# Performance work log

Measured on AMD Instinct MI355X. Metric: run time of the kernel, lower is better.

The kernel has to match this reference:

```python
import jax, jax.numpy as jnp
import numpy as np


def setup_inputs() -> dict:
    key = jax.random.key(0)
    kc, kh, kx, kwx, kwh = jax.random.split(key, 5)
    B, T, D, H = 64, 512, 1024, 1024
    c0 = jax.random.normal(kc, (B, H), dtype=jnp.float32)
    h0 = jax.random.normal(kh, (B, H), dtype=jnp.float32)
    xs = jax.random.normal(kx, (B, T, D), dtype=jnp.float32)
    # fan-in scaled init like lecun_normal (flax default)
    Wx = jax.random.normal(kwx, (D, 4 * H), dtype=jnp.float32) / np.sqrt(D)
    Wh = jax.random.normal(kwh, (H, 4 * H), dtype=jnp.float32) / np.sqrt(H)
    b = jnp.zeros((4 * H,), dtype=jnp.float32)
    return {"c0": c0, "h0": h0, "xs": xs, "Wx": Wx, "Wh": Wh, "b": b}


def _lstm(c0, h0, xs, Wx, Wh, b):
    # Batch the input-to-hidden projection across all timesteps (compute-dense GEMM)
    xproj = jnp.einsum('btd,dh->tbh', xs, Wx)  # [T, B, 4H], time-major for scan

    def step(carry, xp):
        c, h = carry
        gates = xp + h @ Wh + b                # [B, 4H]
        i, f, g, o = jnp.split(gates, 4, axis=-1)  # flax gate order: i, f, g, o
        new_c = jax.nn.sigmoid(f) * c + jax.nn.sigmoid(i) * jnp.tanh(g)
        new_h = jax.nn.sigmoid(o) * jnp.tanh(new_c)
        return (new_c, new_h), new_h

    (cT, hT), ys = jax.lax.scan(step, (c0, h0), xproj)
    return (cT, hT), jnp.transpose(ys, (1, 0, 2))  # ys back to [B, T, H]


def reference(c0, h0, xs, Wx, Wh, b):
    return _lstm(c0, h0, xs, Wx, Wh, b)
```

## Files before the change

### kernel.cpp

```cpp
#include <hip/hip_runtime.h>


typedef _Float16 half8 __attribute__((ext_vector_type(8)));
typedef float floatx4 __attribute__((ext_vector_type(4)));

__device__ __forceinline__ void gll16(const void* g, void* l) {
  __builtin_amdgcn_global_load_lds(
      (const __attribute__((address_space(1))) unsigned int*)g,
      (__attribute__((address_space(3))) unsigned int*)l, 16, 0, 0);
}

__device__ __forceinline__ float sigm(float x) { return 1.f / (1.f + __expf(-x)); }
__device__ __forceinline__ float tanhfast(float x) { return 1.f - 2.f / (__expf(2.f * x) + 1.f); }

__global__ void prep_ew(const float* __restrict__ xs, const float* __restrict__ h0,
                        _Float16* __restrict__ xs16, _Float16* __restrict__ hb0,
                        int* __restrict__ flags) {
  long gid = (long)blockIdx.x * blockDim.x + threadIdx.x;
  if (gid < 4194304) {
    const float4* p = (const float4*)xs + gid * 2;
    float4 u = p[0], w = p[1];
    half8 o;
    o[0] = (_Float16)u.x; o[1] = (_Float16)u.y; o[2] = (_Float16)u.z; o[3] = (_Float16)u.w;
    o[4] = (_Float16)w.x; o[5] = (_Float16)w.y; o[6] = (_Float16)w.z; o[7] = (_Float16)w.w;
    long e = gid * 8;
    long row = e >> 10;
    long b = row >> 9, t = row & 511;
    *(half8*)(xs16 + ((t << 6) + b) * 1024 + (e & 1023)) = o;
  } else if (gid < 4202496) {
    long j = gid - 4194304;
    const float4* p = (const float4*)h0 + j * 2;
    float4 u = p[0], w = p[1];
    half8 o;
    o[0] = (_Float16)u.x; o[1] = (_Float16)u.y; o[2] = (_Float16)u.z; o[3] = (_Float16)u.w;
    o[4] = (_Float16)w.x; o[5] = (_Float16)w.y; o[6] = (_Float16)w.z; o[7] = (_Float16)w.w;
    *(half8*)(hb0 + j * 8) = o;
  } else if (gid < 4203264) {
    flags[gid - 4202496] = 0;
  }
}

__global__ void transpose_k(const float* __restrict__ in, _Float16* __restrict__ outp) {
  __shared__ float s[32][33];
  int bx = blockIdx.x * 32, by = blockIdx.y * 32;
  int tx = threadIdx.x, ty = threadIdx.y;
#pragma unroll
  for (int k = 0; k < 32; k += 8)
    s[ty + k][tx] = in[(long)(by + ty + k) * 4096 + bx + tx];
  __syncthreads();
#pragma unroll
  for (int k = 0; k < 32; k += 8)
    outp[(long)(bx + ty + k) * 1024 + by + tx] = (_Float16)s[tx][ty + k];
}

__global__ __launch_bounds__(256, 1) void fused(const _Float16* __restrict__ xs16,
                                                const _Float16* __restrict__ wxt,
                                                _Float16* __restrict__ xprj,
                                                const _Float16* __restrict__ wht,
                                                const float* __restrict__ bias,
                                                const float* __restrict__ c0,
                                                _Float16* __restrict__ hbuf,
                                                int* __restrict__ flags,
                                                float* __restrict__ out) {
  __shared__ char smem[131072];
  const int tid = threadIdx.x;
  int* const cnt = flags + 256;
  int* const tot = flags + 512;

  if (blockIdx.x >= 64) {
    _Float16* sA = (_Float16*)smem;
    _Float16* sB = (_Float16*)(smem + 8192);
    const int gid = blockIdx.x - 64;
    const int by = gid >> 5, bx = gid & 31;
    const int w = tid >> 6, l = tid & 63, li = l & 15, q = l >> 4;
    const int wr = w >> 1, wc = w & 1;
    const int m0 = by * 128, n0 = bx * 128;
    floatx4 acc[4][4] = {};
    const _Float16* gA0 = xs16 + (long)(m0 + (w * 16 + li)) * 1024 + q * 8;
    const _Float16* gA1 = xs16 + (long)(m0 + ((4 + w) * 16 + li)) * 1024 + q * 8;
    const _Float16* gB0 = wxt + (long)(n0 + (w * 16 + li)) * 1024 + q * 8;
    const _Float16* gB1 = wxt + (long)(n0 + ((4 + w) * 16 + li)) * 1024 + q * 8;
    _Float16* lA0 = sA + (w * 64) * 8;
    _Float16* lA1 = sA + (256 + w * 64) * 8;
    _Float16* lB0 = sB + (w * 64) * 8;
    _Float16* lB1 = sB + (256 + w * 64) * 8;
    for (int k0 = 0; k0 < 1024; k0 += 32) {
      __syncthreads();
      gll16(gA0 + k0, lA0);
      gll16(gA1 + k0, lA1);
      gll16(gB0 + k0, lB0);
      gll16(gB1 + k0, lB1);
      __syncthreads();
      half8 af[4], bf[4];
      const half8* pA = (const half8*)sA;
      const half8* pB = (const half8*)sB;
#pragma unroll
      for (int i = 0; i < 4; i++) af[i] = pA[(wr * 4 + i) * 64 + l];
#pragma unroll
      for (int j = 0; j < 4; j++) bf[j] = pB[(wc * 4 + j) * 64 + l];
#pragma unroll
      for (int i = 0; i < 4; i++)
#pragma unroll
        for (int j = 0; j < 4; j++)
          acc[i][j] = __builtin_amdgcn_mfma_f32_16x16x32_f16(af[i], bf[j], acc[i][j], 0, 0, 0);
    }
#pragma unroll
    for (int i = 0; i < 4; i++) {
#pragma unroll
      for (int r = 0; r < 4; r++) {
        int m = m0 + wr * 64 + i * 16 + q * 4 + r;
#pragma unroll
        for (int j = 0; j < 4; j++) {
          int gn = n0 + wc * 64 + j * 16 + li;
          xprj[(long)m * 4096 + gn] = (_Float16)acc[i][j][r];
        }
      }
    }
    __syncthreads();
    if (tid == 0) {
      __builtin_amdgcn_fence(__ATOMIC_RELEASE, "agent");
      __hip_atomic_fetch_add(&cnt[by], 1, __ATOMIC_RELAXED, __HIP_MEMORY_SCOPE_AGENT);
      __hip_atomic_fetch_add(tot, 1, __ATOMIC_RELAXED, __HIP_MEMORY_SCOPE_AGENT);
    }
    return;
  }

  _Float16* sW = (_Float16*)smem;
  const int wgid = blockIdx.x;
  const int v = tid >> 6;
  const int l = tid & 63, li = l & 15, q = l >> 4;
  const int ks = wgid * 16;

#pragma unroll 4
  for (int i = 0; i < 32; i++) {
    int c = i * 256 + tid;
    int g = c >> 11, kk = (c >> 6) & 31;
    int cli = c & 15, cq = (c >> 4) & 3;
    gll16(wht + (long)((g << 10) + ks + cli) * 1024 + kk * 32 + cq * 8,
          sW + (long)(c - l) * 8);
  }
  float creg[4];
#pragma unroll
  for (int r = 0; r < 4; r++)
    creg[r] = c0[(long)(v * 16 + q * 4 + r) * 1024 + ks + li];
  float bs[4];
#pragma unroll
  for (int g = 0; g < 4; g++) bs[g] = bias[(g << 10) + ks + li];
  __syncthreads();

  const half8* pW = (const half8*)sW;
  const int fidx = 4 * l + v;
  int xdone = 0;

  for (int t = 0; t < 512; t++) {
    if (!xdone && !(t & 1)) {
      const int nb = t >> 1;
      for (;;) {
        int cr = __hip_atomic_load(&cnt[nb], __ATOMIC_RELAXED, __HIP_MEMORY_SCOPE_AGENT);
        if (cr >= 32) break;
        __builtin_amdgcn_s_sleep(16);
      }
      xdone = (__hip_atomic_load(tot, __ATOMIC_RELAXED, __HIP_MEMORY_SCOPE_AGENT) >= 8192);
      __builtin_amdgcn_fence(__ATOMIC_ACQUIRE, "agent");
    }

    const _Float16* xpt = xprj + (long)t * 262144 + ks + li;
    _Float16 xv[4][4];
#pragma unroll
    for (int g = 0; g < 4; g++)
#pragma unroll
      for (int r = 0; r < 4; r++)
        xv[g][r] = xpt[(long)(v * 16 + q * 4 + r) * 4096 + (g << 10)];

    for (;;) {
      int f = __hip_atomic_load(&flags[fidx], __ATOMIC_RELAXED, __HIP_MEMORY_SCOPE_AGENT);
      if (__all(f >= t)) break;
      __builtin_amdgcn_s_sleep(1);
    }
    __builtin_amdgcn_fence(__ATOMIC_ACQUIRE, "workgroup");

    const _Float16* hrow = hbuf + (long)t * 65536 + (long)(v * 16 + li) * 1024 + q * 8;
    floatx4 acc[4] = {};
    half8 ap[8];
#pragma unroll
    for (int p = 0; p < 8; p++) ap[p] = *(const half8*)(hrow + p * 32);
#pragma unroll
    for (int kk = 0; kk < 32; kk++) {
      half8 a = ap[kk & 7];
#pragma unroll
      for (int g = 0; g < 4; g++)
        acc[g] = __builtin_amdgcn_mfma_f32_16x16x32_f16(a, pW[((g * 32 + kk) << 6) + l], acc[g], 0, 0, 0);
      if (kk < 24) ap[kk & 7] = *(const half8*)(hrow + (kk + 8) * 32);
    }

    _Float16* hnext = hbuf + (long)(t + 1) * 65536;
    float hval[4], cval[4];
#pragma unroll
    for (int r = 0; r < 4; r++) {
      float gi = acc[0][r] + (float)xv[0][r] + bs[0];
      float gf = acc[1][r] + (float)xv[1][r] + bs[1];
      float gg = acc[2][r] + (float)xv[2][r] + bs[2];
      float go = acc[3][r] + (float)xv[3][r] + bs[3];
      float cN = sigm(gf) * creg[r] + sigm(gi) * tanhfast(gg);
      creg[r] = cN;
      cval[r] = cN;
      float hN = sigm(go) * tanhfast(cN);
      hval[r] = hN;
      int b = v * 16 + q * 4 + r;
      unsigned short hu = __builtin_bit_cast(unsigned short, (_Float16)hN);
      __hip_atomic_store((unsigned short*)hnext + (long)b * 1024 + ks + li, hu,
                         __ATOMIC_RELAXED, __HIP_MEMORY_SCOPE_AGENT);
    }
    __builtin_amdgcn_s_waitcnt(0);
    if (l == 0)
      __hip_atomic_store(&flags[4 * wgid + v], t + 1, __ATOMIC_RELAXED, __HIP_MEMORY_SCOPE_AGENT);

#pragma unroll
    for (int r = 0; r < 4; r++) {
      int b = v * 16 + q * 4 + r;
      out[131072 + (long)b * 524288 + (long)t * 1024 + ks + li] = hval[r];
      if (t == 511) {
        out[(long)b * 1024 + ks + li] = cval[r];
        out[65536 + (long)b * 1024 + ks + li] = hval[r];
      }
    }
  }
}

extern "C" void kernel_launch(void* const* d_in, const int* in_sizes, int n_in,
                              void* d_out, int out_size, void* d_ws, size_t ws_size,
                              hipStream_t stream) {
  const float* c0 = (const float*)d_in[0];
  const float* h0 = (const float*)d_in[1];
  const float* xs = (const float*)d_in[2];
  const float* Wx = (const float*)d_in[3];
  const float* Wh = (const float*)d_in[4];
  const float* bias = (const float*)d_in[5];
  float* out = (float*)d_out;

  char* ws = (char*)d_ws;
  size_t off = 0;
  _Float16* xs16 = (_Float16*)(ws + off); off += 67108864;
  _Float16* wxt  = (_Float16*)(ws + off); off += 8388608;
  _Float16* wht  = (_Float16*)(ws + off); off += 8388608;
  _Float16* xprj = (_Float16*)(ws + off); off += 268435456;
  _Float16* hbuf = (_Float16*)(ws + off); off += 67239936;
  int* flags     = (int*)(ws + off);      off += 4096;
  if (ws_size < off) return;

  prep_ew<<<16419, 256, 0, stream>>>(xs, h0, xs16, hbuf, flags);
  transpose_k<<<dim3(128, 32), dim3(32, 8), 0, stream>>>(Wx, wxt);
  transpose_k<<<dim3(128, 32), dim3(32, 8), 0, stream>>>(Wh, wht);
  fused<<<8256, 256, 0, stream>>>(xs16, wxt, xprj, wht, bias, c0, hbuf, flags, out);
}
```

Before: 5.930 ms.

## Prefetch next-step input projections and batch all h loads in recurrent loop

```diff
diff --git a/kernel.cpp b/kernel.cpp
--- a/kernel.cpp
+++ b/kernel.cpp
@@ -152,79 +152,100 @@
   const int fidx = 4 * l + v;
   int xdone = 0;
 
-  for (int t = 0; t < 512; t++) {
-    if (!xdone && !(t & 1)) {
-      const int nb = t >> 1;
-      for (;;) {
-        int cr = __hip_atomic_load(&cnt[nb], __ATOMIC_RELAXED, __HIP_MEMORY_SCOPE_AGENT);
-        if (cr >= 32) break;
-        __builtin_amdgcn_s_sleep(16);
-      }
-      xdone = (__hip_atomic_load(tot, __ATOMIC_RELAXED, __HIP_MEMORY_SCOPE_AGENT) >= 8192);
-      __builtin_amdgcn_fence(__ATOMIC_ACQUIRE, "agent");
-    }
-
-    const _Float16* xpt = xprj + (long)t * 262144 + ks + li;
-    _Float16 xv[4][4];
+  for (;;) {
+    int cr = __hip_atomic_load(&cnt[0], __ATOMIC_RELAXED, __HIP_MEMORY_SCOPE_AGENT);
+    if (cr >= 32) break;
+    __builtin_amdgcn_s_sleep(16);
+  }
+  xdone = (__hip_atomic_load(tot, __ATOMIC_RELAXED, __HIP_MEMORY_SCOPE_AGENT) >= 8192);
+  __builtin_amdgcn_fence(__ATOMIC_ACQUIRE, "agent");
+  _Float16 xvA[4][4], xvB[4][4];
+  {
+    const _Float16* xp0 = xprj + ks + li;
 #pragma unroll
     for (int g = 0; g < 4; g++)
 #pragma unroll
       for (int r = 0; r < 4; r++)
-        xv[g][r] = xpt[(long)(v * 16 + q * 4 + r) * 4096 + (g << 10)];
-
-    for (;;) {
-      int f = __hip_atomic_load(&flags[fidx], __ATOMIC_RELAXED, __HIP_MEMORY_SCOPE_AGENT);
-      if (__all(f >= t)) break;
-      __builtin_amdgcn_s_sleep(1);
-    }
-    __builtin_amdgcn_fence(__ATOMIC_ACQUIRE, "workgroup");
-
-    const _Float16* hrow = hbuf + (long)t * 65536 + (long)(v * 16 + li) * 1024 + q * 8;
-    floatx4 acc[4] = {};
-    half8 ap[8];
-#pragma unroll
-    for (int p = 0; p < 8; p++) ap[p] = *(const half8*)(hrow + p * 32);
-#pragma unroll
-    for (int kk = 0; kk < 32; kk++) {
-      half8 a = ap[kk & 7];
-#pragma unroll
-      for (int g = 0; g < 4; g++)
-        acc[g] = __builtin_amdgcn_mfma_f32_16x16x32_f16(a, pW[((g * 32 + kk) << 6) + l], acc[g], 0, 0, 0);
-      if (kk < 24) ap[kk & 7] = *(const half8*)(hrow + (kk + 8) * 32);
-    }
-
-    _Float16* hnext = hbuf + (long)(t + 1) * 65536;
-    float hval[4], cval[4];
-#pragma unroll
-    for (int r = 0; r < 4; r++) {
-      float gi = acc[0][r] + (float)xv[0][r] + bs[0];
-      float gf = acc[1][r] + (float)xv[1][r] + bs[1];
-      float gg = acc[2][r] + (float)xv[2][r] + bs[2];
-      float go = acc[3][r] + (float)xv[3][r] + bs[3];
-      float cN = sigm(gf) * creg[r] + sigm(gi) * tanhfast(gg);
-      creg[r] = cN;
-      cval[r] = cN;
-      float hN = sigm(go) * tanhfast(cN);
-      hval[r] = hN;
-      int b = v * 16 + q * 4 + r;
-      unsigned short hu = __builtin_bit_cast(unsigned short, (_Float16)hN);
-      __hip_atomic_store((unsigned short*)hnext + (long)b * 1024 + ks + li, hu,
-                         __ATOMIC_RELAXED, __HIP_MEMORY_SCOPE_AGENT);
-    }
-    __builtin_amdgcn_s_waitcnt(0);
-    if (l == 0)
-      __hip_atomic_store(&flags[4 * wgid + v], t + 1, __ATOMIC_RELAXED, __HIP_MEMORY_SCOPE_AGENT);
-
-#pragma unroll
-    for (int r = 0; r < 4; r++) {
-      int b = v * 16 + q * 4 + r;
-      out[131072 + (long)b * 524288 + (long)t * 1024 + ks + li] = hval[r];
-      if (t == 511) {
-        out[(long)b * 1024 + ks + li] = cval[r];
-        out[65536 + (long)b * 1024 + ks + li] = hval[r];
-      }
-    }
-  }
+        xvA[g][r] = xp0[(long)(v * 16 + q * 4 + r) * 4096 + (g << 10)];
+  }
+
+#define STEP(T, XC, XN, DOGATE)                                                           \
+  {                                                                                       \
+    const int t_ = (T);                                                                   \
+                           \
+    int f_ = __hip_atomic_load(&flags[fidx], __ATOMIC_RELAXED, __HIP_MEMORY_SCOPE_AGENT); \
+                    \
+    if (DOGATE && (t_ + 1) < 512 && !xdone) {                                             \
+      const int nb_ = (t_ + 1) >> 1;                                                      \
+      for (;;) {                                                                          \
+        int cr_ = __hip_atomic_load(&cnt[nb_], __ATOMIC_RELAXED, __HIP_MEMORY_SCOPE_AGENT); \
+        if (cr_ >= 32) break;                                                             \
+        __builtin_amdgcn_s_sleep(16);                                                     \
+      }                                                                                   \
+      xdone = (__hip_atomic_load(tot, __ATOMIC_RELAXED, __HIP_MEMORY_SCOPE_AGENT) >= 8192); \
+      __builtin_amdgcn_fence(__ATOMIC_ACQUIRE, "agent");                                  \
+    }                                                                                     \
+                          \
+    if ((t_ + 1) < 512) {                                                                 \
+      const _Float16* xpn_ = xprj + (long)(t_ + 1) * 262144 + ks + li;                    \
+      _Pragma("unroll") for (int g = 0; g < 4; g++)                                       \
+        _Pragma("unroll") for (int r = 0; r < 4; r++)                                     \
+          XN[g][r] = xpn_[(long)(v * 16 + q * 4 + r) * 4096 + (g << 10)];                 \
+    }                                                                                     \
+                          \
+    for (;;) {                                                                            \
+      if (__all(f_ >= t_)) break;                                                         \
+      __builtin_amdgcn_s_sleep(1);                                                        \
+      f_ = __hip_atomic_load(&flags[fidx], __ATOMIC_RELAXED, __HIP_MEMORY_SCOPE_AGENT);   \
+    }                                                                                     \
+    __builtin_amdgcn_fence(__ATOMIC_ACQUIRE, "workgroup");                                \
+                                \
+    const _Float16* hrow_ = hbuf + (long)t_ * 65536 + (long)(v * 16 + li) * 1024 + q * 8; \
+    floatx4 acc_[4] = {};                                                                 \
+    half8 ap_[32];                                                                        \
+    _Pragma("unroll") for (int p = 0; p < 32; p++)                                        \
+      ap_[p] = *(const half8*)(hrow_ + p * 32);                                           \
+    _Pragma("unroll") for (int kk = 0; kk < 32; kk++) {                                   \
+      _Pragma("unroll") for (int g = 0; g < 4; g++)                                       \
+        acc_[g] = __builtin_amdgcn_mfma_f32_16x16x32_f16(ap_[kk], pW[((g * 32 + kk) << 6) + l], acc_[g], 0, 0, 0); \
+    }                                                                                     \
+                                               \
+    _Float16* hnext_ = hbuf + (long)(t_ + 1) * 65536;                                     \
+    float hval_[4], cval_[4];                                                             \
+    _Pragma("unroll") for (int r = 0; r < 4; r++) {                                       \
+      float gi = acc_[0][r] + (float)XC[0][r] + bs[0];                                    \
+      float gf = acc_[1][r] + (float)XC[1][r] + bs[1];                                    \
+      float gg = acc_[2][r] + (float)XC[2][r] + bs[2];                                    \
+      float go = acc_[3][r] + (float)XC[3][r] + bs[3];                                    \
+      float cN = sigm(gf) * creg[r] + sigm(gi) * tanhfast(gg);                            \
+      creg[r] = cN;                                                                       \
+      cval_[r] = cN;                                                                      \
+      float hN = sigm(go) * tanhfast(cN);                                                 \
+      hval_[r] = hN;                                                                      \
+      int b_ = v * 16 + q * 4 + r;                                                        \
+      unsigned short hu_ = __builtin_bit_cast(unsigned short, (_Float16)hN);              \
+      __hip_atomic_store((unsigned short*)hnext_ + (long)b_ * 1024 + ks + li, hu_,        \
+                         __ATOMIC_RELAXED, __HIP_MEMORY_SCOPE_AGENT);                     \
+    }                                                                                     \
+    __builtin_amdgcn_s_waitcnt(0);                             \
+    if (l == 0)                                                                           \
+      __hip_atomic_store(&flags[4 * wgid + v], t_ + 1, __ATOMIC_RELAXED, __HIP_MEMORY_SCOPE_AGENT); \
+                                  \
+    _Pragma("unroll") for (int r = 0; r < 4; r++) {                                       \
+      int b_ = v * 16 + q * 4 + r;                                                        \
+      out[131072 + (long)b_ * 524288 + (long)t_ * 1024 + ks + li] = hval_[r];             \
+      if (t_ == 511) {                                                                    \
+        out[(long)b_ * 1024 + ks + li] = cval_[r];                                        \
+        out[65536 + (long)b_ * 1024 + ks + li] = hval_[r];                                \
+      }                                                                                   \
+    }                                                                                     \
+  }
+
+  for (int t2 = 0; t2 < 512; t2 += 2) {
+    STEP(t2, xvA, xvB, 0)
+    STEP(t2 + 1, xvB, xvA, 1)
+  }
+#undef STEP
 }
 
 extern "C" void kernel_launch(void* const* d_in, const int* in_sizes, int n_in,
```

New measurement: 6.105 ms. 1.03x slower.
